# Kernel tuning notes

Hardware: AMD Instinct MI355X
Metric: run time of the kernel (lower is better)

The kernel has to match this reference:

```python
import jax, jax.numpy as jnp
import numpy as np

B, F_SP, F_DN, VOCAB, EMB = 16384, 26, 13, 100000, 16


def setup_inputs() -> dict:
    key = jax.random.key(0)
    ks = jax.random.split(key, 9)
    sparse_inputs = jax.random.randint(ks[0], (B, F_SP), 0, VOCAB, dtype=jnp.int32)
    dense_inputs = jax.random.normal(ks[1], (B, F_DN), dtype=jnp.float32)
    s = 0.02
    return {
        "sparse_inputs": sparse_inputs,
        "dense_inputs": dense_inputs,
        "linear_dense_W": jax.random.normal(ks[2], (F_DN, 1), jnp.float32) * s,
        "linear_dense_b": jnp.zeros((1,), jnp.float32),
        "linear_emb": jax.random.normal(ks[3], (F_SP, VOCAB, 1), jnp.float32) * s,  # per-feature 1-d linear embeddings
        "fm_emb": jax.random.normal(ks[4], (F_SP, VOCAB, EMB), jnp.float32) * s,    # per-feature FM embeddings
        "finish_W": jax.random.normal(ks[5], (1, 1), jnp.float32) * s,
        "finish_b": jnp.zeros((1,), jnp.float32),
        "like_W": jax.random.normal(ks[6], (1, 1), jnp.float32) * s,
        "like_b": jnp.zeros((1,), jnp.float32),
    }


def reference(sparse_inputs, dense_inputs, linear_dense_W, linear_dense_b,
              linear_emb, fm_emb, finish_W, finish_b, like_W, like_b):
    feat_idx = jnp.arange(F_SP)[None, :]  # [1, F]

    # first-order: dense linear + sum of 1-d sparse embeddings
    lin_dense = dense_inputs @ linear_dense_W + linear_dense_b          # [B, 1]
    lin_sparse = linear_emb[feat_idx, sparse_inputs]                    # [B, F, 1]
    first_order = lin_dense + jnp.sum(lin_sparse, axis=1)               # [B, 1]

    # second-order FM: 0.5 * sum((sum_f v)^2 - sum_f v^2)
    emb = fm_emb[feat_idx, sparse_inputs]                               # [B, F, E]
    summed = jnp.sum(emb, axis=1)                                       # [B, E]
    second_order = 0.5 * jnp.sum(summed * summed - jnp.sum(emb * emb, axis=1),
                                 axis=1, keepdims=True)                 # [B, 1]

    logits = first_order + second_order                                 # [B, 1]
    finish = jax.nn.sigmoid(logits @ finish_W + finish_b)               # [B, 1]
    like = jax.nn.sigmoid(logits @ like_W + like_b)                     # [B, 1]
    return jnp.concatenate([finish, like], axis=1)                      # [B, 2]
```

## Files before the change

### kernel.cpp

```cpp
#include <hip/hip_runtime.h>
#include <math.h>

#define B_TOT 16384
#define F_SP  26
#define F_DN  13
#define VOCAB 100000
#define EMB   16

__global__ __launch_bounds__(256) void fm_mtl_kernel(
    const int*   __restrict__ sparse,
    const float* __restrict__ dense,
    const float* __restrict__ ldW,
    const float* __restrict__ ldB,
    const float* __restrict__ lin_emb,
    const float* __restrict__ fm_emb,
    const float* __restrict__ fW,
    const float* __restrict__ fB,
    const float* __restrict__ lW,
    const float* __restrict__ lB,
    float*       __restrict__ out)
{
    __shared__ int s_idx[16 * F_SP];
    const int tid = threadIdx.x;
    const int block_base = blockIdx.x * 16;

    for (int i = tid; i < 16 * F_SP; i += 256)
        s_idx[i] = sparse[block_base * F_SP + i];
    __syncthreads();

    const int sloc = tid >> 4;
    const int g    = tid & 15;
    const int d    = g & 7;
    const int fh   = g >> 3;
    const int b    = block_base + sloc;

    const int* idx = &s_idx[sloc * F_SP];

    float lin = lin_emb[(size_t)g * VOCAB + (size_t)idx[g]];
    if (g < 10)
        lin += lin_emb[(size_t)(g + 16) * VOCAB + (size_t)idx[g + 16]];
    if (g < F_DN)
        lin += dense[b * F_DN + g] * ldW[g];
    if (g == 0)
        lin += ldB[0];

    float2 s = make_float2(0.f, 0.f);
    float ssq = 0.f;
    const int f0 = fh * 13;
    #pragma unroll
    for (int k = 0; k < 13; ++k) {
        const int f = f0 + k;
        const int v = idx[f];
        const float2 e = *reinterpret_cast<const float2*>(
            &fm_emb[((size_t)f * VOCAB + (size_t)v) * EMB + d * 2]);
        s.x += e.x; s.y += e.y;
        ssq += e.x * e.x + e.y * e.y;
    }

    s.x += __shfl_xor(s.x, 8);
    s.y += __shfl_xor(s.y, 8);

    const float p2 = s.x * s.x + s.y * s.y;
    float r = 0.25f * p2 - 0.5f * ssq + lin;
    r += __shfl_xor(r, 1);
    r += __shfl_xor(r, 2);
    r += __shfl_xor(r, 4);
    r += __shfl_xor(r, 8);

    if (g == 0) {
        const float finish = 1.f / (1.f + expf(-(r * fW[0] + fB[0])));
        const float like   = 1.f / (1.f + expf(-(r * lW[0] + lB[0])));
        *reinterpret_cast<float2*>(&out[b * 2]) = make_float2(finish, like);
    }
}

extern "C" void kernel_launch(void* const* d_in, const int* in_sizes, int n_in,
                              void* d_out, int out_size, void* d_ws, size_t ws_size,
                              hipStream_t stream) {
    const int*   sparse  = (const int*)  d_in[0];
    const float* dense   = (const float*)d_in[1];
    const float* ldW     = (const float*)d_in[2];
    const float* ldB     = (const float*)d_in[3];
    const float* lin_emb = (const float*)d_in[4];
    const float* fm_emb  = (const float*)d_in[5];
    const float* fW      = (const float*)d_in[6];
    const float* fB      = (const float*)d_in[7];
    const float* lW      = (const float*)d_in[8];
    const float* lB      = (const float*)d_in[9];
    float* out = (float*)d_out;

    dim3 grid(B_TOT / 16);
    dim3 block(256);
    fm_mtl_kernel<<<grid, block, 0, stream>>>(
        sparse, dense, ldW, ldB, lin_emb, fm_emb, fW, fB, lW, lB, out);
}
```

Baseline: 20.64 us.

## Split FM gather into eight feature-group partial kernel plus finish kernel

Splits the work across two kernels. The first kernel runs eight times as many blocks, each handling a group of 3-4 features per sample. It writes partial embedding sums and scalar terms to a workspace buffer, and a second kernel reduces the partials and applies the sigmoids. The aim is more memory-level parallelism for the random embedding gathers. The cost is a second launch, about 8.5 MB of extra workspace writes and reads, and scalar rather than float2 loads per lane. The original fused kernel is kept as a fallback when the workspace is too small.

```diff
diff --git a/kernel.cpp b/kernel.cpp
--- a/kernel.cpp
+++ b/kernel.cpp
@@ -7,66 +7,142 @@
 #define VOCAB 100000
 #define EMB   16
 
-__global__ __launch_bounds__(256) void fm_mtl_kernel(
+#define S_PART_FLOATS   (8 * B_TOT * EMB)
+#define SC_PART_FLOATS  (8 * B_TOT)
+#define WS_FLOATS       (S_PART_FLOATS + SC_PART_FLOATS)
+
+__global__ __launch_bounds__(256) void fm_partial_kernel(
     const int*   __restrict__ sparse,
+    const float* __restrict__ lin_emb,
+    const float* __restrict__ fm_emb,
+    float*       __restrict__ s_part,
+    float*       __restrict__ sc_part)
+{
+    const int gid   = blockIdx.x;
+    const int g     = gid & 7;
+    const int chunk = gid >> 3;
+    const int tid   = threadIdx.x;
+    const int sloc  = tid >> 4;
+    const int l     = tid & 15;
+    const int b     = chunk * 16 + sloc;
+    const int nf    = (g < 2) ? 4 : 3;
+
+    int myidx = 0;
+    if (l < nf)
+        myidx = sparse[b * F_SP + g + 8 * l];
+
+    const int v0 = __shfl(myidx, 0, 16);
+    const int v1 = __shfl(myidx, 1, 16);
+    const int v2 = __shfl(myidx, 2, 16);
+    const int v3 = __shfl(myidx, 3, 16);
+
+    const float* basep = fm_emb + l;
+    const float e0 = basep[((size_t)(g)      * VOCAB + (size_t)v0) * EMB];
+    const float e1 = basep[((size_t)(g + 8)  * VOCAB + (size_t)v1) * EMB];
+    const float e2 = basep[((size_t)(g + 16) * VOCAB + (size_t)v2) * EMB];
+    float e3 = 0.f;
+    if (nf == 4)
+        e3 = basep[((size_t)(g + 24) * VOCAB + (size_t)v3) * EMB];
+
+    float lin = 0.f;
+    if (l < nf)
+        lin = lin_emb[(size_t)(g + 8 * l) * VOCAB + (size_t)myidx];
+
+    const float s   = e0 + e1 + e2 + e3;
+    const float ssq = e0*e0 + e1*e1 + e2*e2 + e3*e3;
+
+    float t = -0.5f * ssq + lin;
+    t += __shfl_xor(t, 1);
+    t += __shfl_xor(t, 2);
+    t += __shfl_xor(t, 4);
+    t += __shfl_xor(t, 8);
+
+    s_part[(((size_t)g << 14) + b) * EMB + l] = s;
+    if (l == 0)
+        sc_part[((size_t)g << 14) + b] = t;
+}
+
+__global__ __launch_bounds__(256) void fm_finish_kernel(
+    const float* __restrict__ s_part,
+    const float* __restrict__ sc_part,
     const float* __restrict__ dense,
     const float* __restrict__ ldW,
     const float* __restrict__ ldB,
-    const float* __restrict__ lin_emb,
-    const float* __restrict__ fm_emb,
-    const float* __restrict__ fW,
-    const float* __restrict__ fB,
-    const float* __restrict__ lW,
-    const float* __restrict__ lB,
+    const float* __restrict__ fW, const float* __restrict__ fB,
+    const float* __restrict__ lW, const float* __restrict__ lB,
     float*       __restrict__ out)
+{
+    const int tid  = threadIdx.x;
+    const int sloc = tid >> 4;
+    const int l    = tid & 15;
+    const int b    = blockIdx.x * 16 + sloc;
+
+    float s = 0.f;
+    #pragma unroll
+    for (int g = 0; g < 8; ++g)
+        s += s_part[(((size_t)g << 14) + b) * EMB + l];
+
+    float t = 0.5f * s * s;
+    if (l < 8)
+        t += sc_part[((size_t)l << 14) + b];
+    if (l < F_DN)
+        t += dense[b * F_DN + l] * ldW[l];
+    if (l == 0)
+        t += ldB[0];
+
+    t += __shfl_xor(t, 1);
+    t += __shfl_xor(t, 2);
+    t += __shfl_xor(t, 4);
+    t += __shfl_xor(t, 8);
+
+    if (l == 0) {
+        const float finish = 1.f / (1.f + expf(-(t * fW[0] + fB[0])));
+        const float like   = 1.f / (1.f + expf(-(t * lW[0] + lB[0])));
+        *reinterpret_cast<float2*>(&out[b * 2]) = make_float2(finish, like);
+    }
+}
+
+__global__ __launch_bounds__(256) void fm_mtl_kernel(
+    const int*   __restrict__ sparse, const float* __restrict__ dense,
+    const float* __restrict__ ldW, const float* __restrict__ ldB,
+    const float* __restrict__ lin_emb, const float* __restrict__ fm_emb,
+    const float* __restrict__ fW, const float* __restrict__ fB,
+    const float* __restrict__ lW, const float* __restrict__ lB,
+    float* __restrict__ out)
 {
     __shared__ int s_idx[16 * F_SP];
     const int tid = threadIdx.x;
     const int block_base = blockIdx.x * 16;
-
     for (int i = tid; i < 16 * F_SP; i += 256)
         s_idx[i] = sparse[block_base * F_SP + i];
     __syncthreads();
 
-    const int sloc = tid >> 4;
-    const int g    = tid & 15;
-    const int d    = g & 7;
-    const int fh   = g >> 3;
-    const int b    = block_base + sloc;
-
+    const int sloc = tid >> 4, g = tid & 15, d = g & 7, fh = g >> 3;
+    const int b = block_base + sloc;
     const int* idx = &s_idx[sloc * F_SP];
 
     float lin = lin_emb[(size_t)g * VOCAB + (size_t)idx[g]];
-    if (g < 10)
-        lin += lin_emb[(size_t)(g + 16) * VOCAB + (size_t)idx[g + 16]];
-    if (g < F_DN)
-        lin += dense[b * F_DN + g] * ldW[g];
-    if (g == 0)
-        lin += ldB[0];
+    if (g < 10) lin += lin_emb[(size_t)(g + 16) * VOCAB + (size_t)idx[g + 16]];
+    if (g < F_DN) lin += dense[b * F_DN + g] * ldW[g];
+    if (g == 0) lin += ldB[0];
 
     float2 s = make_float2(0.f, 0.f);
     float ssq = 0.f;
     const int f0 = fh * 13;
     #pragma unroll
     for (int k = 0; k < 13; ++k) {
-        const int f = f0 + k;
-        const int v = idx[f];
+        const int f = f0 + k, v = idx[f];
         const float2 e = *reinterpret_cast<const float2*>(
             &fm_emb[((size_t)f * VOCAB + (size_t)v) * EMB + d * 2]);
         s.x += e.x; s.y += e.y;
         ssq += e.x * e.x + e.y * e.y;
     }
-
     s.x += __shfl_xor(s.x, 8);
     s.y += __shfl_xor(s.y, 8);
-
     const float p2 = s.x * s.x + s.y * s.y;
     float r = 0.25f * p2 - 0.5f * ssq + lin;
-    r += __shfl_xor(r, 1);
-    r += __shfl_xor(r, 2);
-    r += __shfl_xor(r, 4);
-    r += __shfl_xor(r, 8);
-
+    r += __shfl_xor(r, 1); r += __shfl_xor(r, 2);
+    r += __shfl_xor(r, 4); r += __shfl_xor(r, 8);
     if (g == 0) {
         const float finish = 1.f / (1.f + expf(-(r * fW[0] + fB[0])));
         const float like   = 1.f / (1.f + expf(-(r * lW[0] + lB[0])));
@@ -89,8 +165,15 @@
     const float* lB      = (const float*)d_in[9];
     float* out = (float*)d_out;
 
-    dim3 grid(B_TOT / 16);
-    dim3 block(256);
-    fm_mtl_kernel<<<grid, block, 0, stream>>>(
-        sparse, dense, ldW, ldB, lin_emb, fm_emb, fW, fB, lW, lB, out);
+    if (ws_size >= (size_t)WS_FLOATS * sizeof(float)) {
+        float* s_part  = (float*)d_ws;
+        float* sc_part = s_part + S_PART_FLOATS;
+        fm_partial_kernel<<<dim3(8 * (B_TOT / 16)), dim3(256), 0, stream>>>(
+            sparse, lin_emb, fm_emb, s_part, sc_part);
+        fm_finish_kernel<<<dim3(B_TOT / 16), dim3(256), 0, stream>>>(
+            s_part, sc_part, dense, ldW, ldB, fW, fB, lW, lB, out);
+    } else {
+        fm_mtl_kernel<<<dim3(B_TOT / 16), dim3(256), 0, stream>>>(
+            sparse, dense, ldW, ldB, lin_emb, fm_emb, fW, fB, lW, lB, out);
+    }
 }
```

Result: slower. 22.96 us (+11.3%).

## Split linear-embedding gather into separate pre-pass kernel writing workspace partials

Applied to the files above, without the earlier changes.

Moves the first-order sparse linear-embedding lookups into a new kernel. Each block handles 64 samples for a subset of features, so gathers for one feature come from the same table slice, and the kernel writes 8 partial sums per sample to the workspace. The main FM kernel then reads those partials instead of issuing scattered lin_emb loads. This adds a second launch and a workspace round trip, and falls back to the fused kernel when the workspace is too small.

```diff
diff --git a/kernel.cpp b/kernel.cpp
--- a/kernel.cpp
+++ b/kernel.cpp
@@ -7,17 +7,50 @@
 #define VOCAB 100000
 #define EMB   16
 
-__global__ __launch_bounds__(256) void fm_mtl_kernel(
+#define WS_FLOATS (B_TOT * 8)
+
+__global__ __launch_bounds__(256) void lin_partial_kernel(
+    const int*   __restrict__ sparse,
+    const float* __restrict__ lin_emb,
+    float*       __restrict__ t_lin)
+{
+    __shared__ int   s_idx[64 * F_SP];
+    __shared__ float part[4][64];
+
+    const int g     = blockIdx.x & 7;
+    const int chunk = blockIdx.x >> 3;
+    const int tid   = threadIdx.x;
+    const int w     = tid >> 6;
+    const int l     = tid & 63;
+    const int b0    = chunk * 64;
+
+    for (int i = tid; i < 64 * F_SP; i += 256)
+        s_idx[i] = sparse[b0 * F_SP + i];
+    __syncthreads();
+
+    const int f = g + 8 * w;
+    float v = 0.f;
+    if (f < F_SP) {
+        const int idx = s_idx[l * F_SP + f];
+        v = lin_emb[(size_t)f * VOCAB + (size_t)idx];
+    }
+    part[w][l] = v;
+    __syncthreads();
+
+    if (w == 0)
+        t_lin[(size_t)(b0 + l) * 8 + g] =
+            part[0][l] + part[1][l] + part[2][l] + part[3][l];
+}
+
+__global__ __launch_bounds__(256) void fm_main_kernel(
     const int*   __restrict__ sparse,
     const float* __restrict__ dense,
     const float* __restrict__ ldW,
     const float* __restrict__ ldB,
-    const float* __restrict__ lin_emb,
     const float* __restrict__ fm_emb,
-    const float* __restrict__ fW,
-    const float* __restrict__ fB,
-    const float* __restrict__ lW,
-    const float* __restrict__ lB,
+    const float* __restrict__ t_lin,
+    const float* __restrict__ fW, const float* __restrict__ fB,
+    const float* __restrict__ lW, const float* __restrict__ lB,
     float*       __restrict__ out)
 {
     __shared__ int s_idx[16 * F_SP];
@@ -33,12 +66,11 @@
     const int d    = g & 7;
     const int fh   = g >> 3;
     const int b    = block_base + sloc;
-
     const int* idx = &s_idx[sloc * F_SP];
 
-    float lin = lin_emb[(size_t)g * VOCAB + (size_t)idx[g]];
-    if (g < 10)
-        lin += lin_emb[(size_t)(g + 16) * VOCAB + (size_t)idx[g + 16]];
+    float lin = 0.f;
+    if (g < 8)
+        lin = t_lin[(size_t)b * 8 + g];
     if (g < F_DN)
         lin += dense[b * F_DN + g] * ldW[g];
     if (g == 0)
@@ -74,6 +106,54 @@
     }
 }
 
+__global__ __launch_bounds__(256) void fm_mtl_kernel(
+    const int*   __restrict__ sparse, const float* __restrict__ dense,
+    const float* __restrict__ ldW, const float* __restrict__ ldB,
+    const float* __restrict__ lin_emb, const float* __restrict__ fm_emb,
+    const float* __restrict__ fW, const float* __restrict__ fB,
+    const float* __restrict__ lW, const float* __restrict__ lB,
+    float* __restrict__ out)
+{
+    __shared__ int s_idx[16 * F_SP];
+    const int tid = threadIdx.x;
+    const int block_base = blockIdx.x * 16;
+    for (int i = tid; i < 16 * F_SP; i += 256)
+        s_idx[i] = sparse[block_base * F_SP + i];
+    __syncthreads();
+
+    const int sloc = tid >> 4, g = tid & 15, d = g & 7, fh = g >> 3;
+    const int b = block_base + sloc;
+    const int* idx = &s_idx[sloc * F_SP];
+
+    float lin = lin_emb[(size_t)g * VOCAB + (size_t)idx[g]];
+    if (g < 10) lin += lin_emb[(size_t)(g + 16) * VOCAB + (size_t)idx[g + 16]];
+    if (g < F_DN) lin += dense[b * F_DN + g] * ldW[g];
+    if (g == 0) lin += ldB[0];
+
+    float2 s = make_float2(0.f, 0.f);
+    float ssq = 0.f;
+    const int f0 = fh * 13;
+    #pragma unroll
+    for (int k = 0; k < 13; ++k) {
+        const int f = f0 + k, v = idx[f];
+        const float2 e = *reinterpret_cast<const float2*>(
+            &fm_emb[((size_t)f * VOCAB + (size_t)v) * EMB + d * 2]);
+        s.x += e.x; s.y += e.y;
+        ssq += e.x * e.x + e.y * e.y;
+    }
+    s.x += __shfl_xor(s.x, 8);
+    s.y += __shfl_xor(s.y, 8);
+    const float p2 = s.x * s.x + s.y * s.y;
+    float r = 0.25f * p2 - 0.5f * ssq + lin;
+    r += __shfl_xor(r, 1); r += __shfl_xor(r, 2);
+    r += __shfl_xor(r, 4); r += __shfl_xor(r, 8);
+    if (g == 0) {
+        const float finish = 1.f / (1.f + expf(-(r * fW[0] + fB[0])));
+        const float like   = 1.f / (1.f + expf(-(r * lW[0] + lB[0])));
+        *reinterpret_cast<float2*>(&out[b * 2]) = make_float2(finish, like);
+    }
+}
+
 extern "C" void kernel_launch(void* const* d_in, const int* in_sizes, int n_in,
                               void* d_out, int out_size, void* d_ws, size_t ws_size,
                               hipStream_t stream) {
@@ -89,8 +169,14 @@
     const float* lB      = (const float*)d_in[9];
     float* out = (float*)d_out;
 
-    dim3 grid(B_TOT / 16);
-    dim3 block(256);
-    fm_mtl_kernel<<<grid, block, 0, stream>>>(
-        sparse, dense, ldW, ldB, lin_emb, fm_emb, fW, fB, lW, lB, out);
+    if (ws_size >= (size_t)WS_FLOATS * sizeof(float)) {
+        float* t_lin = (float*)d_ws;
+        lin_partial_kernel<<<dim3(8 * (B_TOT / 64)), dim3(256), 0, stream>>>(
+            sparse, lin_emb, t_lin);
+        fm_main_kernel<<<dim3(B_TOT / 16), dim3(256), 0, stream>>>(
+            sparse, dense, ldW, ldB, fm_emb, t_lin, fW, fB, lW, lB, out);
+    } else {
+        fm_mtl_kernel<<<dim3(B_TOT / 16), dim3(256), 0, stream>>>(
+            sparse, dense, ldW, ldB, lin_emb, fm_emb, fW, fB, lW, lB, out);
+    }
 }
```

New measurement: 23.42 us. 13.5% more time.
